# Kernel tuning notes

Measured on AMD Instinct MI355X. Metric: run time of the kernel, lower is better.

The kernel has to match this reference:

```python
import jax, jax.numpy as jnp
import numpy as np

N_VERTS = 100000
N_HYPEREDGES = 10000
N_INC = 1600000   # incidence pairs (vertex, hyperedge)
N_EDGES = 1600000 # graph edges
C_IN = 256
C_OUT = 64
NEG_SLOPE = 0.2


def setup_inputs() -> dict:
    key = jax.random.key(0)
    ks = jax.random.split(key, 10)
    x = jax.random.normal(ks[0], (N_VERTS, C_IN), dtype=jnp.float32)
    hg_v = jax.random.randint(ks[1], (N_INC,), 0, N_VERTS)
    hg_e = jax.random.randint(ks[2], (N_INC,), 0, N_HYPEREDGES)
    g_src = jax.random.randint(ks[3], (N_EDGES,), 0, N_VERTS)
    g_dst = jax.random.randint(ks[4], (N_EDGES,), 0, N_VERTS)
    # theta: Linear(C_in, C_in//2) -> LeakyReLU(0.2) -> Linear(C_in//2, C_out)
    s1 = 1.0 / np.sqrt(C_IN)
    s2 = 1.0 / np.sqrt(C_IN // 2)
    W1 = jax.random.uniform(ks[5], (C_IN, C_IN // 2), jnp.float32, -s1, s1)
    b1 = jax.random.uniform(ks[6], (C_IN // 2,), jnp.float32, -s1, s1)
    W2 = jax.random.uniform(ks[7], (C_IN // 2, C_OUT), jnp.float32, -s2, s2)
    b2 = jax.random.uniform(ks[8], (C_OUT,), jnp.float32, -s2, s2)
    w = jnp.ones((2,), dtype=jnp.float32)
    return {"x": x, "W1": W1, "b1": b1, "W2": W2, "b2": b2, "w": w,
            "hg_v": hg_v, "hg_e": hg_e, "g_src": g_src, "g_dst": g_dst,
            "n_hyperedges": N_HYPEREDGES}


def _mean_seg(vals, idx, num_segments):
    # segment mean with zero-degree guard
    s = jax.ops.segment_sum(vals, idx, num_segments=num_segments)
    d = jax.ops.segment_sum(jnp.ones((idx.shape[0],), vals.dtype), idx,
                            num_segments=num_segments)
    return s / jnp.maximum(d, 1.0)[:, None]


def reference(x, W1, b1, W2, b2, w, hg_v, hg_e, g_src, g_dst, n_hyperedges):
    n = x.shape[0]
    sw = jax.nn.softmax(w)  # w1 = e^{w0}/sum, w2 = e^{w1}/sum
    # theta MLP (is_last=False path)
    h = jax.nn.leaky_relu(x @ W1 + b1, NEG_SLOPE) @ W2 + b2  # [N, C_out]
    # hypergraph v2v mean: v2e mean then e2v mean over incidence pairs
    e_feat = _mean_seg(h[hg_v], hg_e, n_hyperedges)          # [E_hg, C_out]
    x_hg = _mean_seg(e_feat[hg_e], hg_v, n)                  # [N, C_out]
    # graph v2v mean: per-vertex mean over neighbors
    x_g = _mean_seg(h[g_src], g_dst, n)                      # [N, C_out]
    x_fuse = (x_g + x_hg) * 0.5
    out = sw[0] * x_fuse + sw[1] * h
    # use_bn=False -> no BN; eval-mode dropout is identity
    out = jax.nn.leaky_relu(out, NEG_SLOPE)
    return out
```

## Files before the change

kernel.cpp:

```cpp
#include <hip/hip_runtime.h>
#include <hip/hip_bf16.h>
#include <hip/hip_fp16.h>

#define N_VERTS   100000
#define N_HGE     10000
#define N_INC     1600000
#define N_EDGES   1600000
#define C_IN      256
#define C_MID     128
#define C_OUT     64
#define NEG       0.2f

#define EBSHIFT 6
#define NB_E    157
#define VBSHIFT 9
#define NB_V    196
#define NB_MAX  196
#define ECAP    12288
#define VCAP    10240
#define PAIRS_PER_BLOCK 4096
#define QP 16

typedef __attribute__((ext_vector_type(8))) _Float16 f16x8;
typedef __attribute__((ext_vector_type(4))) float    f32x4;

__device__ __forceinline__ unsigned packh2(float a, float b) {
    const __half2 h = __float22half2_rn(make_float2(a, b));
    return *(const unsigned*)&h;
}
__device__ __forceinline__ ushort h1bits(float v) {
    const __half x = __float2half_rn(v);
    return *(const ushort*)&x;
}

__device__ __forceinline__ void h8acc(float4& a0, float4& a1, uint4 p) {
    const float2 f0 = __half22float2(*(__half2*)&p.x);
    const float2 f1 = __half22float2(*(__half2*)&p.y);
    const float2 f2 = __half22float2(*(__half2*)&p.z);
    const float2 f3 = __half22float2(*(__half2*)&p.w);
    a0.x += f0.x; a0.y += f0.y; a0.z += f1.x; a0.w += f1.y;
    a1.x += f2.x; a1.y += f2.y; a1.z += f3.x; a1.w += f3.y;
}

__device__ __forceinline__ void xreduce8(float4& a, float4& b) {
#pragma unroll
    for (int m = 8; m <= 32; m <<= 1) {
        a.x += __shfl_xor(a.x, m); a.y += __shfl_xor(a.y, m);
        a.z += __shfl_xor(a.z, m); a.w += __shfl_xor(a.w, m);
        b.x += __shfl_xor(b.x, m); b.y += __shfl_xor(b.y, m);
        b.z += __shfl_xor(b.z, m); b.w += __shfl_xor(b.w, m);
    }
}

__global__ __launch_bounds__(256) void
prep_w_kernel(const float* __restrict__ W1, const float* __restrict__ W2,
              ushort* __restrict__ W1t, ushort* __restrict__ W2t) {
    const int idx = blockIdx.x * 256 + threadIdx.x;
    if (idx < C_IN * C_MID) {
        const int n = idx >> 8, k = idx & 255;
        W1t[idx] = h1bits(W1[k * C_MID + n]);
    } else {
        const int j = idx - C_IN * C_MID;
        if (j < C_MID * C_OUT) {
            const int n = j >> 7, k = j & 127;
            W2t[j] = h1bits(W2[k * C_OUT + n]);
        }
    }
}

#define MBM 128
__global__ __launch_bounds__(512) void
mlp_mfma_kernel(const float* __restrict__ x,
                const ushort* __restrict__ W1t, const ushort* __restrict__ W2t,
                const float* __restrict__ b1, const float* __restrict__ b2,
                __half* __restrict__ h) {
    __shared__ ushort buf[18432];
    ushort* xs  = buf;
    ushort* ws  = buf + 9216;
    ushort* mid = buf;

    const int t    = threadIdx.x;
    const int lane = t & 63;
    const int wid  = t >> 6;
    const int wr   = wid >> 2, wc = wid & 3;
    const int v0   = blockIdx.x * MBM;
    const int rem  = N_VERTS - v0;
    const int l15  = lane & 15;
    const int lg   = lane >> 4;

    f32x4 acc[4][2];
#pragma unroll
    for (int i = 0; i < 4; ++i) { acc[i][0] = (f32x4)0.f; acc[i][1] = (f32x4)0.f; }

    for (int kt = 0; kt < 4; ++kt) {
        __syncthreads();
#pragma unroll
        for (int it = 0; it < 4; ++it) {
            const int idx = it * 512 + t;
            const int row = idx >> 4;
            const int c4  = (idx & 15) * 4;
            float4 v = make_float4(0.f, 0.f, 0.f, 0.f);
            if (row < rem)
                v = *(const float4*)&x[(size_t)(v0 + row) * C_IN + kt * 64 + c4];
            uint2 p;
            p.x = packh2(v.x, v.y);
            p.y = packh2(v.z, v.w);
            *(uint2*)&xs[row * 72 + c4] = p;
        }
#pragma unroll
        for (int it = 0; it < 4; ++it) {
            const int idx = it * 512 + t;
            const int n  = idx >> 4;
            const int c4 = (idx & 15) * 4;
            *(uint2*)&ws[n * 72 + c4] = *(const uint2*)&W1t[n * 256 + kt * 64 + c4];
        }
        __syncthreads();

#pragma unroll
        for (int ks = 0; ks < 2; ++ks) {
            const int k0 = ks * 32 + lg * 8;
            f16x8 a[4], b[2];
#pragma unroll
            for (int mf = 0; mf < 4; ++mf)
                a[mf] = *(const f16x8*)&xs[(wr * 64 + mf * 16 + l15) * 72 + k0];
#pragma unroll
            for (int nf = 0; nf < 2; ++nf)
                b[nf] = *(const f16x8*)&ws[(wc * 32 + nf * 16 + l15) * 72 + k0];
#pragma unroll
            for (int mf = 0; mf < 4; ++mf)
#pragma unroll
                for (int nf = 0; nf < 2; ++nf)
                    acc[mf][nf] = __builtin_amdgcn_mfma_f32_16x16x32_f16(
                        a[mf], b[nf], acc[mf][nf], 0, 0, 0);
        }
    }
    __syncthreads();

#pragma unroll
    for (int nf = 0; nf < 2; ++nf) {
        const int col = wc * 32 + nf * 16 + l15;
        const float bias = b1[col];
#pragma unroll
        for (int mf = 0; mf < 4; ++mf)
#pragma unroll
            for (int j = 0; j < 4; ++j) {
                const int r = wr * 64 + mf * 16 + lg * 4 + j;
                float v = acc[mf][nf][j] + bias;
                v = v > 0.f ? v : NEG * v;
                mid[r * 136 + col] = h1bits(v);
            }
    }
    __syncthreads();

    f32x4 acc2[4];
#pragma unroll
    for (int i = 0; i < 4; ++i) acc2[i] = (f32x4)0.f;

#pragma unroll
    for (int ks2 = 0; ks2 < 4; ++ks2) {
        const int k0 = ks2 * 32 + lg * 8;
        f16x8 a[4];
#pragma unroll
        for (int mf = 0; mf < 4; ++mf)
            a[mf] = *(const f16x8*)&mid[(wr * 64 + mf * 16 + l15) * 136 + k0];
        const f16x8 b = *(const f16x8*)&W2t[(wc * 16 + l15) * 128 + k0];
#pragma unroll
        for (int mf = 0; mf < 4; ++mf)
            acc2[mf] = __builtin_amdgcn_mfma_f32_16x16x32_f16(
                a[mf], b, acc2[mf], 0, 0, 0);
    }

    {
        const int col = wc * 16 + l15;
        const float b2c = b2[col];
#pragma unroll
        for (int mf = 0; mf < 4; ++mf)
#pragma unroll
            for (int j = 0; j < 4; ++j) {
                const int r = wr * 64 + mf * 16 + lg * 4 + j;
                if (r < rem)
                    h[(size_t)(v0 + r) * C_OUT + col] =
                        __float2half_rn(acc2[mf][j] + b2c);
            }
    }
}

__global__ __launch_bounds__(256) void
partitionA_kernel(const int* __restrict__ hg_v, const int* __restrict__ hg_e,
                  const int* __restrict__ g_src, const int* __restrict__ g_dst,
                  int* __restrict__ bcur_e, int* __restrict__ bcur_vhg,
                  int* __restrict__ bcur_vg,
                  unsigned* __restrict__ rec_e, unsigned* __restrict__ rec_vhg,
                  unsigned* __restrict__ rec_vg) {
    __shared__ int hist[NB_MAX];
    __shared__ int lstart[NB_MAX];
    __shared__ int gb[NB_MAX];
    __shared__ int sscan[256];
    __shared__ unsigned lbuf[PAIRS_PER_BLOCK];
    __shared__ unsigned char bkt8[PAIRS_PER_BLOCK];
    const int t    = threadIdx.x;
    const int i0   = blockIdx.x * PAIRS_PER_BLOCK;
    const int vcnt = min(PAIRS_PER_BLOCK, N_INC - i0);

    for (int table = 0; table < 3; ++table) {
        const int *dsts, *pays; int *bcur; unsigned* rec; int shift, nb, cap;
        if (table == 0)      { dsts = hg_e;  pays = hg_v;  bcur = bcur_e;
                               rec = rec_e;   shift = EBSHIFT; nb = NB_E; cap = ECAP; }
        else if (table == 1) { dsts = hg_v;  pays = hg_e;  bcur = bcur_vhg;
                               rec = rec_vhg; shift = VBSHIFT; nb = NB_V; cap = VCAP; }
        else                 { dsts = g_dst; pays = g_src; bcur = bcur_vg;
                               rec = rec_vg;  shift = VBSHIFT; nb = NB_V; cap = VCAP; }
        const int dmask = (1 << shift) - 1;

        if (t < nb) hist[t] = 0;
        __syncthreads();

        unsigned pk[QP]; int bk[QP], rk[QP];
#pragma unroll
        for (int q = 0; q < QP; ++q) {
            const int i = i0 + t + q * 256;
            if (i < N_INC) {
                const int d = dsts[i];
                const int p = pays[i];
                bk[q] = d >> shift;
                pk[q] = ((unsigned)(d & dmask) << 17) | (unsigned)p;
                rk[q] = atomicAdd(&hist[bk[q]], 1);
            } else bk[q] = -1;
        }
        __syncthreads();

        {
            const int own = (t < nb) ? hist[t] : 0;
            sscan[t] = own;
            __syncthreads();
            for (int d2 = 1; d2 < 256; d2 <<= 1) {
                int v = (t >= d2) ? sscan[t - d2] : 0;
                __syncthreads();
                sscan[t] += v;
                __syncthreads();
            }
            if (t < nb) {
                lstart[t] = sscan[t] - own;
                gb[t] = own ? atomicAdd(&bcur[t], own) : 0;
            }
        }
        __syncthreads();

#pragma unroll
        for (int q = 0; q < QP; ++q) {
            if (bk[q] >= 0) {
                const int lp = lstart[bk[q]] + rk[q];
                lbuf[lp] = pk[q];
                bkt8[lp] = (unsigned char)bk[q];
            }
        }
        __syncthreads();

        for (int i = t; i < vcnt; i += 256) {
            const int b  = bkt8[i];
            const int pos = gb[b] + (i - lstart[b]);
            if (pos < cap)
                rec[(size_t)b * cap + pos] = lbuf[i];
        }
        __syncthreads();
    }
}

#define GRID_B (NB_E + 2 * NB_V)
__global__ __launch_bounds__(256) void
partitionB_kernel(unsigned* __restrict__ rec_e, unsigned* __restrict__ rec_vhg,
                  unsigned* __restrict__ rec_vg,
                  const int* __restrict__ bcur_e, const int* __restrict__ bcur_vhg,
                  const int* __restrict__ bcur_vg,
                  int* __restrict__ deg_e, int* __restrict__ deg_vhg,
                  int* __restrict__ deg_vg,
                  int* __restrict__ off_e, int* __restrict__ off_vhg,
                  int* __restrict__ off_vg) {
    __shared__ int slotbuf[ECAP];
    __shared__ int cnt_l[1 << VBSHIFT];
    __shared__ int cur_l[1 << VBSHIFT];
    __shared__ int part[256];

    int blk = blockIdx.x;
    unsigned* rec; const int* bcur; int* deg; int* off;
    int b, shift, ndst, cap;
    if (blk < NB_E) {
        rec = rec_e; bcur = bcur_e; deg = deg_e; off = off_e;
        shift = EBSHIFT; ndst = N_HGE; cap = ECAP; b = blk;
    } else if (blk < NB_E + NB_V) {
        rec = rec_vhg; bcur = bcur_vhg; deg = deg_vhg; off = off_vhg;
        shift = VBSHIFT; ndst = N_VERTS; cap = VCAP; b = blk - NB_E;
    } else {
        rec = rec_vg; bcur = bcur_vg; deg = deg_vg; off = off_vg;
        shift = VBSHIFT; ndst = N_VERTS; cap = VCAP; b = blk - NB_E - NB_V;
    }
    const int t    = threadIdx.x;
    const int dlo  = b << shift;
    const int nd   = 1 << shift;
    const int ndc  = min(nd, ndst - dlo);
    const int bs   = b * cap;
    const int bcnt = min(bcur[b], cap);

    for (int j = t; j < nd; j += 256) cnt_l[j] = 0;
    __syncthreads();
    for (int i = t; i < bcnt; i += 256)
        atomicAdd(&cnt_l[rec[bs + i] >> 17], 1);
    __syncthreads();

    const int chunk = (nd + 255) / 256;
    const int lo = t * chunk;
    const int hi = min(lo + chunk, nd);
    int s = 0;
    for (int j = lo; j < hi; ++j) s += cnt_l[j];
    part[t] = s;
    __syncthreads();
    for (int d = 1; d < 256; d <<= 1) {
        int v = (t >= d) ? part[t - d] : 0;
        __syncthreads();
        part[t] += v;
        __syncthreads();
    }
    int run = (t > 0) ? part[t - 1] : 0;
    for (int j = lo; j < hi; ++j) { cur_l[j] = run; run += cnt_l[j]; }
    __syncthreads();

    for (int j = t; j < ndc; j += 256) {
        deg[dlo + j] = cnt_l[j];
        off[dlo + j] = bs + cur_l[j];
    }
    __syncthreads();

    for (int i = t; i < bcnt; i += 256) {
        const unsigned r = rec[bs + i];
        const int lpos = atomicAdd(&cur_l[r >> 17], 1);
        slotbuf[lpos] = (int)(r & 0x1FFFFu);
    }
    __syncthreads();
    for (int i = t; i < bcnt; i += 256)
        rec[bs + i] = (unsigned)slotbuf[i];
}

__global__ void gather_e_kernel(const int* __restrict__ slot, const int* __restrict__ off,
                                const int* __restrict__ deg, const __half* __restrict__ h,
                                __half* __restrict__ e_feat) {
    const int wid  = (blockIdx.x * blockDim.x + threadIdx.x) >> 6;
    const int lane = threadIdx.x & 63;
    if (wid >= N_HGE) return;
    const int sub = lane >> 3;
    const int cp  = lane & 7;
    const int n    = deg[wid];
    const int base = off[wid];

    float4 a0 = make_float4(0.f, 0.f, 0.f, 0.f);
    float4 a1 = make_float4(0.f, 0.f, 0.f, 0.f);
    int j = 0;
    for (; j + 16 <= n; j += 16) {
        const int s0 = slot[base + j + sub];
        const int s1 = slot[base + j + 8 + sub];
        const uint4 p0 = *(const uint4*)&h[(unsigned)(s0 * C_OUT + 8 * cp)];
        const uint4 p1 = *(const uint4*)&h[(unsigned)(s1 * C_OUT + 8 * cp)];
        h8acc(a0, a1, p0);
        h8acc(a0, a1, p1);
    }
    for (; j < n; j += 8) {
        const int idx = j + sub;
        const int s = slot[base + (idx < n ? idx : 0)];
        const uint4 p = *(const uint4*)&h[(unsigned)(s * C_OUT + 8 * cp)];
        if (idx < n) h8acc(a0, a1, p);
    }
    xreduce8(a0, a1);
    const float inv = 1.f / fmaxf((float)n, 1.f);
    if (sub == 0) {
        const __half2 r0 = __float22half2_rn(make_float2(a0.x * inv, a0.y * inv));
        const __half2 r1 = __float22half2_rn(make_float2(a0.z * inv, a0.w * inv));
        const __half2 r2 = __float22half2_rn(make_float2(a1.x * inv, a1.y * inv));
        const __half2 r3 = __float22half2_rn(make_float2(a1.z * inv, a1.w * inv));
        uint4 pk;
        pk.x = *(const unsigned*)&r0;
        pk.y = *(const unsigned*)&r1;
        pk.z = *(const unsigned*)&r2;
        pk.w = *(const unsigned*)&r3;
        *(uint4*)&e_feat[(unsigned)(wid * C_OUT + 8 * cp)] = pk;
    }
}

__global__ void vertex_out_kernel(const int* __restrict__ slot_vhg,
                                  const int* __restrict__ off_vhg,
                                  const int* __restrict__ deg_vhg,
                                  const int* __restrict__ slot_vg,
                                  const int* __restrict__ off_vg,
                                  const int* __restrict__ deg_vg,
                                  const __half* __restrict__ e_feat,
                                  const __half* __restrict__ h,
                                  const float* __restrict__ w,
                                  float* __restrict__ out) {
    const int wid  = (blockIdx.x * blockDim.x + threadIdx.x) >> 6;
    const int lane = threadIdx.x & 63;
    if (wid >= N_VERTS) return;
    const int sub = lane >> 3;
    const int cp  = lane & 7;

    float4 hg0 = make_float4(0.f, 0.f, 0.f, 0.f);
    float4 hg1 = make_float4(0.f, 0.f, 0.f, 0.f);
    float inv_hg;
    {
        const int n = deg_vhg[wid];
        const int base = off_vhg[wid];
        int j = 0;
        for (; j + 16 <= n; j += 16) {
            const int s0 = slot_vhg[base + j + sub];
            const int s1 = slot_vhg[base + j + 8 + sub];
            const uint4 p0 = *(const uint4*)&e_feat[(unsigned)(s0 * C_OUT + 8 * cp)];
            const uint4 p1 = *(const uint4*)&e_feat[(unsigned)(s1 * C_OUT + 8 * cp)];
            h8acc(hg0, hg1, p0);
            h8acc(hg0, hg1, p1);
        }
        for (; j < n; j += 8) {
            const int idx = j + sub;
            const int s = slot_vhg[base + (idx < n ? idx : 0)];
            const uint4 p = *(const uint4*)&e_feat[(unsigned)(s * C_OUT + 8 * cp)];
            if (idx < n) h8acc(hg0, hg1, p);
        }
        inv_hg = 1.f / fmaxf((float)n, 1.f);
    }

    float4 g0 = make_float4(0.f, 0.f, 0.f, 0.f);
    float4 g1 = make_float4(0.f, 0.f, 0.f, 0.f);
    float inv_g;
    {
        const int n = deg_vg[wid];
        const int base = off_vg[wid];
        int j = 0;
        for (; j + 16 <= n; j += 16) {
            const int s0 = slot_vg[base + j + sub];
            const int s1 = slot_vg[base + j + 8 + sub];
            const uint4 p0 = *(const uint4*)&h[(unsigned)(s0 * C_OUT + 8 * cp)];
            const uint4 p1 = *(const uint4*)&h[(unsigned)(s1 * C_OUT + 8 * cp)];
            h8acc(g0, g1, p0);
            h8acc(g0, g1, p1);
        }
        for (; j < n; j += 8) {
            const int idx = j + sub;
            const int s = slot_vg[base + (idx < n ? idx : 0)];
            const uint4 p = *(const uint4*)&h[(unsigned)(s * C_OUT + 8 * cp)];
            if (idx < n) h8acc(g0, g1, p);
        }
        inv_g = 1.f / fmaxf((float)n, 1.f);
    }

    xreduce8(hg0, hg1);
    xreduce8(g0, g1);

    const float w0 = w[0], w1 = w[1];
    const float m  = fmaxf(w0, w1);
    const float e0 = __expf(w0 - m), e1 = __expf(w1 - m);
    const float sw0 = e0 / (e0 + e1), sw1 = e1 / (e0 + e1);
    const float c0 = sw0 * 0.5f;

    float4 hv0 = make_float4(0.f, 0.f, 0.f, 0.f);
    float4 hv1 = make_float4(0.f, 0.f, 0.f, 0.f);
    h8acc(hv0, hv1, *(const uint4*)&h[(unsigned)(wid * C_OUT + 8 * cp)]);

    float4 o0, o1;
    o0.x = c0 * (g0.x * inv_g + hg0.x * inv_hg) + sw1 * hv0.x;
    o0.y = c0 * (g0.y * inv_g + hg0.y * inv_hg) + sw1 * hv0.y;
    o0.z = c0 * (g0.z * inv_g + hg0.z * inv_hg) + sw1 * hv0.z;
    o0.w = c0 * (g0.w * inv_g + hg0.w * inv_hg) + sw1 * hv0.w;
    o1.x = c0 * (g1.x * inv_g + hg1.x * inv_hg) + sw1 * hv1.x;
    o1.y = c0 * (g1.y * inv_g + hg1.y * inv_hg) + sw1 * hv1.y;
    o1.z = c0 * (g1.z * inv_g + hg1.z * inv_hg) + sw1 * hv1.z;
    o1.w = c0 * (g1.w * inv_g + hg1.w * inv_hg) + sw1 * hv1.w;
    o0.x = o0.x > 0.f ? o0.x : NEG * o0.x;
    o0.y = o0.y > 0.f ? o0.y : NEG * o0.y;
    o0.z = o0.z > 0.f ? o0.z : NEG * o0.z;
    o0.w = o0.w > 0.f ? o0.w : NEG * o0.w;
    o1.x = o1.x > 0.f ? o1.x : NEG * o1.x;
    o1.y = o1.y > 0.f ? o1.y : NEG * o1.y;
    o1.z = o1.z > 0.f ? o1.z : NEG * o1.z;
    o1.w = o1.w > 0.f ? o1.w : NEG * o1.w;

    if (sub == 0) {
        *(float4*)&out[(unsigned)(wid * C_OUT + 8 * cp)]     = o0;
        *(float4*)&out[(unsigned)(wid * C_OUT + 8 * cp + 4)] = o1;
    }
}

extern "C" void kernel_launch(void* const* d_in, const int* in_sizes, int n_in,
                              void* d_out, int out_size, void* d_ws, size_t ws_size,
                              hipStream_t stream) {
    const float* x    = (const float*)d_in[0];
    const float* W1   = (const float*)d_in[1];
    const float* b1   = (const float*)d_in[2];
    const float* W2   = (const float*)d_in[3];
    const float* b2   = (const float*)d_in[4];
    const float* w    = (const float*)d_in[5];
    const int*  hg_v  = (const int*)d_in[6];
    const int*  hg_e  = (const int*)d_in[7];
    const int*  g_src = (const int*)d_in[8];
    const int*  g_dst = (const int*)d_in[9];
    float* out = (float*)d_out;

    unsigned* rec_e   = (unsigned*)d_ws;
    unsigned* rec_vhg = rec_e   + (size_t)NB_E * ECAP;
    unsigned* rec_vg  = rec_vhg + (size_t)NB_V * VCAP;
    int* bcur_e    = (int*)(rec_vg + (size_t)NB_V * VCAP);
    int* bcur_vhg  = bcur_e   + NB_E;
    int* bcur_vg   = bcur_vhg + NB_V;
    int* deg_e     = bcur_vg  + NB_V;
    int* deg_vhg   = deg_e    + N_HGE;
    int* deg_vg    = deg_vhg  + N_VERTS;
    int* off_e     = deg_vg   + N_VERTS;
    int* off_vhg   = off_e    + N_HGE;
    int* off_vg    = off_vhg  + N_VERTS;
    uintptr_t hp   = ((uintptr_t)(off_vg + N_VERTS) + 255) & ~(uintptr_t)255;
    __half* h      = (__half*)hp;
    __half* e_feat = h + (size_t)N_VERTS * C_OUT;
    ushort* W1t    = (ushort*)(e_feat + (size_t)N_HGE * C_OUT);
    ushort* W2t    = W1t + C_IN * C_MID;

    hipMemsetAsync(bcur_e, 0, (NB_E + 2 * NB_V) * sizeof(int), stream);

    const int partA_blocks = (N_INC + PAIRS_PER_BLOCK - 1) / PAIRS_PER_BLOCK;
    partitionA_kernel<<<partA_blocks, 256, 0, stream>>>(
        hg_v, hg_e, g_src, g_dst, bcur_e, bcur_vhg, bcur_vg,
        rec_e, rec_vhg, rec_vg);
    partitionB_kernel<<<GRID_B, 256, 0, stream>>>(
        rec_e, rec_vhg, rec_vg, bcur_e, bcur_vhg, bcur_vg,
        deg_e, deg_vhg, deg_vg, off_e, off_vhg, off_vg);

    prep_w_kernel<<<(C_IN * C_MID + C_MID * C_OUT + 255) / 256, 256, 0, stream>>>(
        W1, W2, W1t, W2t);

    mlp_mfma_kernel<<<(N_VERTS + MBM - 1) / MBM, 512, 0, stream>>>(
        x, W1t, W2t, b1, b2, h);

    const int ge_blocks = (int)(((size_t)N_HGE * 64 + 255) / 256);
    gather_e_kernel<<<ge_blocks, 256, 0, stream>>>((const int*)rec_e, off_e, deg_e,
                                                   h, e_feat);

    const int vo_blocks = (int)(((size_t)N_VERTS * 64 + 255) / 256);
    vertex_out_kernel<<<vo_blocks, 256, 0, stream>>>(
        (const int*)rec_vhg, off_vhg, deg_vhg,
        (const int*)rec_vg,  off_vg,  deg_vg,
        e_feat, h, w, out);
}
```

Before: 390.9 us.

## Map one segment per 8-lane group instead of per wavefront in gathers

Each 8-lane subgroup now owns one hyperedge or vertex and loops over its neighbors serially with a 4-way unroll, instead of a whole wavefront splitting neighbors across subgroups. This removes the cross-lane shuffle reductions and the partially idle stores, and packs 8 segments per wavefront. In exchange, segments with many neighbors (hyperedges average ~160) become long serial chains. The hyperedge gather then has far fewer active wavefronts, which may reduce latency hiding.

```diff
diff --git a/kernel.cpp b/kernel.cpp
--- a/kernel.cpp
+++ b/kernel.cpp
@@ -40,16 +40,6 @@
     const float2 f3 = __half22float2(*(__half2*)&p.w);
     a0.x += f0.x; a0.y += f0.y; a0.z += f1.x; a0.w += f1.y;
     a1.x += f2.x; a1.y += f2.y; a1.z += f3.x; a1.w += f3.y;
-}
-
-__device__ __forceinline__ void xreduce8(float4& a, float4& b) {
-#pragma unroll
-    for (int m = 8; m <= 32; m <<= 1) {
-        a.x += __shfl_xor(a.x, m); a.y += __shfl_xor(a.y, m);
-        a.z += __shfl_xor(a.z, m); a.w += __shfl_xor(a.w, m);
-        b.x += __shfl_xor(b.x, m); b.y += __shfl_xor(b.y, m);
-        b.z += __shfl_xor(b.z, m); b.w += __shfl_xor(b.w, m);
-    }
 }
 
 __global__ __launch_bounds__(256) void
@@ -343,45 +333,45 @@
 __global__ void gather_e_kernel(const int* __restrict__ slot, const int* __restrict__ off,
                                 const int* __restrict__ deg, const __half* __restrict__ h,
                                 __half* __restrict__ e_feat) {
-    const int wid  = (blockIdx.x * blockDim.x + threadIdx.x) >> 6;
+    const int wv   = (blockIdx.x * blockDim.x + threadIdx.x) >> 6;
     const int lane = threadIdx.x & 63;
-    if (wid >= N_HGE) return;
-    const int sub = lane >> 3;
-    const int cp  = lane & 7;
-    const int n    = deg[wid];
-    const int base = off[wid];
+    const int sub  = lane >> 3;
+    const int cp   = lane & 7;
+    const int eid  = wv * 8 + sub;
+    if (eid >= N_HGE) return;
+    const int n    = deg[eid];
+    const int base = off[eid];
 
     float4 a0 = make_float4(0.f, 0.f, 0.f, 0.f);
     float4 a1 = make_float4(0.f, 0.f, 0.f, 0.f);
     int j = 0;
-    for (; j + 16 <= n; j += 16) {
-        const int s0 = slot[base + j + sub];
-        const int s1 = slot[base + j + 8 + sub];
+    for (; j + 4 <= n; j += 4) {
+        const int s0 = slot[base + j + 0];
+        const int s1 = slot[base + j + 1];
+        const int s2 = slot[base + j + 2];
+        const int s3 = slot[base + j + 3];
         const uint4 p0 = *(const uint4*)&h[(unsigned)(s0 * C_OUT + 8 * cp)];
         const uint4 p1 = *(const uint4*)&h[(unsigned)(s1 * C_OUT + 8 * cp)];
-        h8acc(a0, a1, p0);
-        h8acc(a0, a1, p1);
-    }
-    for (; j < n; j += 8) {
-        const int idx = j + sub;
-        const int s = slot[base + (idx < n ? idx : 0)];
-        const uint4 p = *(const uint4*)&h[(unsigned)(s * C_OUT + 8 * cp)];
-        if (idx < n) h8acc(a0, a1, p);
-    }
-    xreduce8(a0, a1);
+        const uint4 p2 = *(const uint4*)&h[(unsigned)(s2 * C_OUT + 8 * cp)];
+        const uint4 p3 = *(const uint4*)&h[(unsigned)(s3 * C_OUT + 8 * cp)];
+        h8acc(a0, a1, p0); h8acc(a0, a1, p1);
+        h8acc(a0, a1, p2); h8acc(a0, a1, p3);
+    }
+    for (; j < n; ++j) {
+        const int s = slot[base + j];
+        h8acc(a0, a1, *(const uint4*)&h[(unsigned)(s * C_OUT + 8 * cp)]);
+    }
     const float inv = 1.f / fmaxf((float)n, 1.f);
-    if (sub == 0) {
-        const __half2 r0 = __float22half2_rn(make_float2(a0.x * inv, a0.y * inv));
-        const __half2 r1 = __float22half2_rn(make_float2(a0.z * inv, a0.w * inv));
-        const __half2 r2 = __float22half2_rn(make_float2(a1.x * inv, a1.y * inv));
-        const __half2 r3 = __float22half2_rn(make_float2(a1.z * inv, a1.w * inv));
-        uint4 pk;
-        pk.x = *(const unsigned*)&r0;
-        pk.y = *(const unsigned*)&r1;
-        pk.z = *(const unsigned*)&r2;
-        pk.w = *(const unsigned*)&r3;
-        *(uint4*)&e_feat[(unsigned)(wid * C_OUT + 8 * cp)] = pk;
-    }
+    const __half2 r0 = __float22half2_rn(make_float2(a0.x * inv, a0.y * inv));
+    const __half2 r1 = __float22half2_rn(make_float2(a0.z * inv, a0.w * inv));
+    const __half2 r2 = __float22half2_rn(make_float2(a1.x * inv, a1.y * inv));
+    const __half2 r3 = __float22half2_rn(make_float2(a1.z * inv, a1.w * inv));
+    uint4 pk;
+    pk.x = *(const unsigned*)&r0;
+    pk.y = *(const unsigned*)&r1;
+    pk.z = *(const unsigned*)&r2;
+    pk.w = *(const unsigned*)&r3;
+    *(uint4*)&e_feat[(unsigned)(eid * C_OUT + 8 * cp)] = pk;
 }
 
 __global__ void vertex_out_kernel(const int* __restrict__ slot_vhg,
@@ -394,32 +384,35 @@
                                   const __half* __restrict__ h,
                                   const float* __restrict__ w,
                                   float* __restrict__ out) {
-    const int wid  = (blockIdx.x * blockDim.x + threadIdx.x) >> 6;
+    const int wv   = (blockIdx.x * blockDim.x + threadIdx.x) >> 6;
     const int lane = threadIdx.x & 63;
-    if (wid >= N_VERTS) return;
-    const int sub = lane >> 3;
-    const int cp  = lane & 7;
+    const int sub  = lane >> 3;
+    const int cp   = lane & 7;
+    const int vid  = wv * 8 + sub;
+    if (vid >= N_VERTS) return;
 
     float4 hg0 = make_float4(0.f, 0.f, 0.f, 0.f);
     float4 hg1 = make_float4(0.f, 0.f, 0.f, 0.f);
     float inv_hg;
     {
-        const int n = deg_vhg[wid];
-        const int base = off_vhg[wid];
+        const int n = deg_vhg[vid];
+        const int base = off_vhg[vid];
         int j = 0;
-        for (; j + 16 <= n; j += 16) {
-            const int s0 = slot_vhg[base + j + sub];
-            const int s1 = slot_vhg[base + j + 8 + sub];
+        for (; j + 4 <= n; j += 4) {
+            const int s0 = slot_vhg[base + j + 0];
+            const int s1 = slot_vhg[base + j + 1];
+            const int s2 = slot_vhg[base + j + 2];
+            const int s3 = slot_vhg[base + j + 3];
             const uint4 p0 = *(const uint4*)&e_feat[(unsigned)(s0 * C_OUT + 8 * cp)];
             const uint4 p1 = *(const uint4*)&e_feat[(unsigned)(s1 * C_OUT + 8 * cp)];
-            h8acc(hg0, hg1, p0);
-            h8acc(hg0, hg1, p1);
-        }
-        for (; j < n; j += 8) {
-            const int idx = j + sub;
-            const int s = slot_vhg[base + (idx < n ? idx : 0)];
-            const uint4 p = *(const uint4*)&e_feat[(unsigned)(s * C_OUT + 8 * cp)];
-            if (idx < n) h8acc(hg0, hg1, p);
+            const uint4 p2 = *(const uint4*)&e_feat[(unsigned)(s2 * C_OUT + 8 * cp)];
+            const uint4 p3 = *(const uint4*)&e_feat[(unsigned)(s3 * C_OUT + 8 * cp)];
+            h8acc(hg0, hg1, p0); h8acc(hg0, hg1, p1);
+            h8acc(hg0, hg1, p2); h8acc(hg0, hg1, p3);
+        }
+        for (; j < n; ++j) {
+            const int s = slot_vhg[base + j];
+            h8acc(hg0, hg1, *(const uint4*)&e_feat[(unsigned)(s * C_OUT + 8 * cp)]);
         }
         inv_hg = 1.f / fmaxf((float)n, 1.f);
     }
@@ -428,28 +421,27 @@
     float4 g1 = make_float4(0.f, 0.f, 0.f, 0.f);
     float inv_g;
     {
-        const int n = deg_vg[wid];
-        const int base = off_vg[wid];
+        const int n = deg_vg[vid];
+        const int base = off_vg[vid];
         int j = 0;
-        for (; j + 16 <= n; j += 16) {
-            const int s0 = slot_vg[base + j + sub];
-            const int s1 = slot_vg[base + j + 8 + sub];
+        for (; j + 4 <= n; j += 4) {
+            const int s0 = slot_vg[base + j + 0];
+            const int s1 = slot_vg[base + j + 1];
+            const int s2 = slot_vg[base + j + 2];
+            const int s3 = slot_vg[base + j + 3];
             const uint4 p0 = *(const uint4*)&h[(unsigned)(s0 * C_OUT + 8 * cp)];
             const uint4 p1 = *(const uint4*)&h[(unsigned)(s1 * C_OUT + 8 * cp)];
-            h8acc(g0, g1, p0);
-            h8acc(g0, g1, p1);
-        }
-        for (; j < n; j += 8) {
-            const int idx = j + sub;
-            const int s = slot_vg[base + (idx < n ? idx : 0)];
-            const uint4 p = *(const uint4*)&h[(unsigned)(s * C_OUT + 8 * cp)];
-            if (idx < n) h8acc(g0, g1, p);
+            const uint4 p2 = *(const uint4*)&h[(unsigned)(s2 * C_OUT + 8 * cp)];
+            const uint4 p3 = *(const uint4*)&h[(unsigned)(s3 * C_OUT + 8 * cp)];
+            h8acc(g0, g1, p0); h8acc(g0, g1, p1);
+            h8acc(g0, g1, p2); h8acc(g0, g1, p3);
+        }
+        for (; j < n; ++j) {
+            const int s = slot_vg[base + j];
+            h8acc(g0, g1, *(const uint4*)&h[(unsigned)(s * C_OUT + 8 * cp)]);
         }
         inv_g = 1.f / fmaxf((float)n, 1.f);
     }
-
-    xreduce8(hg0, hg1);
-    xreduce8(g0, g1);
 
     const float w0 = w[0], w1 = w[1];
     const float m  = fmaxf(w0, w1);
@@ -459,7 +451,7 @@
 
     float4 hv0 = make_float4(0.f, 0.f, 0.f, 0.f);
     float4 hv1 = make_float4(0.f, 0.f, 0.f, 0.f);
-    h8acc(hv0, hv1, *(const uint4*)&h[(unsigned)(wid * C_OUT + 8 * cp)]);
+    h8acc(hv0, hv1, *(const uint4*)&h[(unsigned)(vid * C_OUT + 8 * cp)]);
 
     float4 o0, o1;
     o0.x = c0 * (g0.x * inv_g + hg0.x * inv_hg) + sw1 * hv0.x;
@@ -479,10 +471,8 @@
     o1.z = o1.z > 0.f ? o1.z : NEG * o1.z;
     o1.w = o1.w > 0.f ? o1.w : NEG * o1.w;
 
-    if (sub == 0) {
-        *(float4*)&out[(unsigned)(wid * C_OUT + 8 * cp)]     = o0;
-        *(float4*)&out[(unsigned)(wid * C_OUT + 8 * cp + 4)] = o1;
-    }
+    *(float4*)&out[(unsigned)(vid * C_OUT + 8 * cp)]     = o0;
+    *(float4*)&out[(unsigned)(vid * C_OUT + 8 * cp + 4)] = o1;
 }
 
 extern "C" void kernel_launch(void* const* d_in, const int* in_sizes, int n_in,
@@ -534,12 +524,12 @@
     mlp_mfma_kernel<<<(N_VERTS + MBM - 1) / MBM, 512, 0, stream>>>(
         x, W1t, W2t, b1, b2, h);
 
-    const int ge_blocks = (int)(((size_t)N_HGE * 64 + 255) / 256);
-    gather_e_kernel<<<ge_blocks, 256, 0, stream>>>((const int*)rec_e, off_e, deg_e,
-                                                   h, e_feat);
-
-    const int vo_blocks = (int)(((size_t)N_VERTS * 64 + 255) / 256);
-    vertex_out_kernel<<<vo_blocks, 256, 0, stream>>>(
+    const int ge_threads = ((N_HGE + 7) / 8) * 64;
+    gather_e_kernel<<<(ge_threads + 255) / 256, 256, 0, stream>>>(
+        (const int*)rec_e, off_e, deg_e, h, e_feat);
+
+    const int vo_threads = ((N_VERTS + 7) / 8) * 64;
+    vertex_out_kernel<<<(vo_threads + 255) / 256, 256, 0, stream>>>(
         (const int*)rec_vhg, off_vhg, deg_vhg,
         (const int*)rec_vg,  off_vg,  deg_vg,
         e_feat, h, w, out);
```

Result: faster. 375.6 us (-3.9%).
